# Optimization experiments

Hardware: AMD Instinct MI355X
Metric: run time of the kernel (lower is better)

## Reference

```python
import jax, jax.numpy as jnp
import numpy as np

N_HEADS = 16
HEAD_K = 128
HEAD_V = 128
SCALE_BASE = 512.0
THETA_BASE = 10000.0


def xpos_tables(seq_len, head_size):
    # Faithful to the torch xpos module with start=0, end=seq_len (no cache)
    alpha = 0.4 * head_size
    drange = np.arange(2, head_size + 2, 2, dtype=np.float32)
    theta = np.repeat((1.0 / THETA_BASE) ** (drange / head_size), 2)  # [head_size]
    zeta = np.repeat((drange / (head_size / 2) + alpha) / (1 + alpha), 2)  # [head_size]
    half = seq_len // 2
    seq = (np.arange(-half, seq_len - half, dtype=np.float32) / SCALE_BASE)[:, None, None]  # [S,1,1]
    c = np.cos(seq * theta[None, None, :])  # [S,1,head_size]
    s = np.sin(seq * theta[None, None, :])
    t = zeta[None, None, :] ** seq
    return jnp.asarray(c), jnp.asarray(s), jnp.asarray(t), jnp.asarray(1.0 / t)


def rotate_every_two(x):
    return jnp.stack((-x[..., 1::2], x[..., 0::2]), axis=-1).reshape(x.shape)


def setup_inputs() -> dict:
    key = jax.random.key(0)
    ks = jax.random.split(key, 5)
    B, S, E = 2, 2048, 2048
    return {
        "activations": jax.random.normal(ks[0], (B, S, E), dtype=jnp.float32),
        "Wq": 0.02 * jax.random.normal(ks[1], (N_HEADS * HEAD_K, E), dtype=jnp.float32),
        "Wk": 0.02 * jax.random.normal(ks[2], (N_HEADS * HEAD_K, E), dtype=jnp.float32),
        "Wv": 0.02 * jax.random.normal(ks[3], (N_HEADS * HEAD_V, E), dtype=jnp.float32),
        "Wo": 0.02 * jax.random.normal(ks[4], (E, N_HEADS * HEAD_V), dtype=jnp.float32),
    }


def reference(activations, Wq, Wk, Wv, Wo):
    B, S, E = activations.shape
    # QKV projections (torch Linear: y = x @ W.T), split heads
    q = (activations @ Wq.T).reshape(B, S, N_HEADS, HEAD_K)
    k = (activations @ Wk.T).reshape(B, S, N_HEADS, HEAD_K)
    v = (activations @ Wv.T).reshape(B, S, N_HEADS, HEAD_V)
    # xpos rotary + scale; tables have shape [S,1,head] broadcasting over heads
    c, s, t, invt = xpos_tables(S, HEAD_K)
    q = (q * c + rotate_every_two(q) * s) * t
    k = (k * c + rotate_every_two(k) * s) * invt
    # causal scaled dot-product attention
    scale = 1.0 / jnp.sqrt(jnp.float32(HEAD_K))
    scores = jnp.einsum("bqhd,bkhd->bhqk", q, k) * scale  # [B,H,S,S]
    causal = jnp.tril(jnp.ones((S, S), dtype=bool))
    scores = jnp.where(causal, scores, jnp.float32(-1e30))
    probs = jax.nn.softmax(scores, axis=-1)
    out = jnp.einsum("bhqk,bkhd->bqhd", probs, v).reshape(B, S, N_HEADS * HEAD_V)
    # down projection (dropout_rate=0 / eval mode)
    return out @ Wo.T
```

## Files before the change

### kernel.cpp

```cpp
#include <hip/hip_runtime.h>
#include <hip/hip_bf16.h>

typedef __attribute__((ext_vector_type(8))) short bf16x8;
typedef __attribute__((ext_vector_type(4))) float f32x4;
typedef __attribute__((ext_vector_type(4))) _Float16 f16x4;
typedef __attribute__((ext_vector_type(8))) _Float16 f16x8;
typedef __attribute__((ext_vector_type(4))) unsigned short u16x4;

#define B_ 2
#define S_ 2048
#define E_ 2048
#define H_ 16
#define D_ 128
#define ELEMS (B_*S_*E_)
#define WELEMS (E_*E_)

__device__ __forceinline__ unsigned short f2bf(float x) {
  unsigned int u = __float_as_uint(x);
  u += 0x7fffu + ((u >> 16) & 1u);
  return (unsigned short)(u >> 16);
}

__device__ __forceinline__ void async_load16(const void* g, void* l) {
  __builtin_amdgcn_global_load_lds(
      (const __attribute__((address_space(1))) unsigned int*)g,
      (__attribute__((address_space(3))) unsigned int*)l, 16, 0, 0);
}

__global__ __launch_bounds__(256)
void cvt_f32_bf16(const float* __restrict__ src, unsigned short* __restrict__ dst, int n4)
{
  const int i = blockIdx.x * 256 + threadIdx.x;
  if (i < n4) {
    const f32x4 v = ((const f32x4*)src)[i];
    u16x4 o;
    o.x = f2bf(v.x); o.y = f2bf(v.y); o.z = f2bf(v.z); o.w = f2bf(v.w);
    ((u16x4*)dst)[i] = o;
  }
}

__global__ __launch_bounds__(256)
void cvt4_f32_bf16(const float* __restrict__ s0, const float* __restrict__ s1,
                   const float* __restrict__ s2, const float* __restrict__ s3,
                   unsigned short* __restrict__ d0, unsigned short* __restrict__ d1,
                   unsigned short* __restrict__ d2, unsigned short* __restrict__ d3,
                   int n4)
{
  const int i = blockIdx.x * 256 + threadIdx.x;
  if (i >= n4) return;
  const float* s; unsigned short* d;
  switch (blockIdx.y) {
    case 0: s = s0; d = d0; break;
    case 1: s = s1; d = d1; break;
    case 2: s = s2; d = d2; break;
    default: s = s3; d = d3; break;
  }
  const f32x4 v = ((const f32x4*)s)[i];
  u16x4 o;
  o.x = f2bf(v.x); o.y = f2bf(v.y); o.z = f2bf(v.z); o.w = f2bf(v.w);
  ((u16x4*)d)[i] = o;
}

template<int OUTMODE>
__global__ __launch_bounds__(256)
void gemm_bt(const __hip_bfloat16* __restrict__ A,
             const __hip_bfloat16* __restrict__ Bw,
             void* __restrict__ C, int M, int N, int K)
{
  __shared__ __hip_bfloat16 As[128*32];
  __shared__ __hip_bfloat16 Bs[128*32];
  const int tid  = threadIdx.x;
  const int lane = tid & 63;
  const int w    = tid >> 6;
  const int m0 = blockIdx.y * 128;
  const int n0 = blockIdx.x * 128;
  const int wm = (w >> 1) * 64;
  const int wn = (w & 1) * 64;
  const int lrow = lane >> 2;
  const int lcol = (lane & 3) * 8;
  const int fr = lane & 15;
  const int fg = lane >> 4;

  f32x4 acc[4][4];
#pragma unroll
  for (int i = 0; i < 4; i++)
#pragma unroll
    for (int j = 0; j < 4; j++) acc[i][j] = (f32x4)0.0f;

  for (int k0 = 0; k0 < K; k0 += 32) {
    __syncthreads();
#pragma unroll
    for (int s = 0; s < 2; s++) {
      const int rbase = s*64 + w*16;
      async_load16(A  + (size_t)(m0 + rbase + lrow)*K + k0 + lcol, As + rbase*32);
      async_load16(Bw + (size_t)(n0 + rbase + lrow)*K + k0 + lcol, Bs + rbase*32);
    }
    __syncthreads();
    bf16x8 af[4], bfr[4];
#pragma unroll
    for (int i = 0; i < 4; i++) {
      af[i]  = *(const bf16x8*)(As + (wm + i*16 + fr)*32 + fg*8);
      bfr[i] = *(const bf16x8*)(Bs + (wn + i*16 + fr)*32 + fg*8);
    }
#pragma unroll
    for (int i = 0; i < 4; i++)
#pragma unroll
      for (int j = 0; j < 4; j++)
        acc[i][j] = __builtin_amdgcn_mfma_f32_16x16x32_bf16(af[i], bfr[j], acc[i][j], 0, 0, 0);
  }

#pragma unroll
  for (int i = 0; i < 4; i++) {
    const int row = m0 + wm + i*16 + fg*4;
#pragma unroll
    for (int j = 0; j < 4; j++) {
      const int col = n0 + wn + j*16 + fr;
#pragma unroll
      for (int r = 0; r < 4; r++) {
        if (OUTMODE == 1) {
          ((float*)C)[(size_t)(row + r)*N + col] = acc[i][j][r];
        } else if (OUTMODE == 0) {
          ((unsigned short*)C)[(size_t)(row + r)*N + col] = f2bf(acc[i][j][r]);
        } else if (OUTMODE == 2) {
          const int rr = row + r;
          const int b = rr >> 11, s = rr & 2047;
          const int h = col >> 7, d = col & 127;
          ((unsigned short*)C)[(((size_t)(b*H_ + h) << 11) + s)*D_ + d] = f2bf(acc[i][j][r]);
        } else {
          const int rr = row + r;
          const int b = rr >> 11, s = rr & 2047;
          const int t = col >> 11;
          const int h = (col >> 7) & 15, d = col & 127;
          ((unsigned short*)C)[(size_t)t*ELEMS +
              (((size_t)(b*H_ + h) << 11) + s)*D_ + d] = f2bf(acc[i][j][r]);
        }
      }
    }
  }
}

__global__ __launch_bounds__(256)
void xpos_rotary(__hip_bfloat16* __restrict__ Q, __hip_bfloat16* __restrict__ Kt)
{
  const int idx = blockIdx.x * 256 + threadIdx.x;
  const int j = idx & 63;
  const int s = (idx >> 6) & 2047;
  const float seq = (float)(s - 1024) * (1.0f/512.0f);
  const float dr = 2.0f + 2.0f*(float)j;
  const float theta = expf(dr * (1.0f/128.0f) * -9.210340371976184f);
  const float zeta  = (dr * (1.0f/64.0f) + 51.2f) * (1.0f/52.2f);
  const float ang = seq * theta;
  const float c  = cosf(ang);
  const float sn = sinf(ang);
  const float t  = expf(seq * logf(zeta));
  const float it = 1.0f / t;

  const size_t base = (size_t)(idx >> 6) * 128 + 2*j;
  unsigned short* Qs = (unsigned short*)Q;
  unsigned short* Ks = (unsigned short*)Kt;
  const float q0 = __bfloat162float(Q[base]),  q1 = __bfloat162float(Q[base+1]);
  Qs[base]   = f2bf((q0*c - q1*sn) * t);
  Qs[base+1] = f2bf((q1*c + q0*sn) * t);
  const float k0 = __bfloat162float(Kt[base]), k1 = __bfloat162float(Kt[base+1]);
  Ks[base]   = f2bf((k0*c - k1*sn) * it);
  Ks[base+1] = f2bf((k1*c + k0*sn) * it);
}

__global__ __launch_bounds__(256)
void transpose_v(const __hip_bfloat16* __restrict__ Vh, _Float16* __restrict__ VT3)
{
  __shared__ float tile[32][33];
  const int tx = threadIdx.x, ty = threadIdx.y;
  const int bh = blockIdx.z;
  const int s0 = blockIdx.x * 32, d0 = blockIdx.y * 32;
  const int kt = s0 >> 6, koff = s0 & 63;
#pragma unroll
  for (int r = 0; r < 4; r++) {
    const int s = s0 + ty + r*8;
    tile[ty + r*8][tx] = __bfloat162float(Vh[((size_t)bh*S_ + s)*D_ + d0 + tx]);
  }
  __syncthreads();
  const int key = koff + tx;
  const int g = (key >> 2) & 3, rr = key & 3, half = (key >> 5) & 1, s1 = (key >> 4) & 1;
  const size_t base = (size_t)bh*S_*D_ + (size_t)kt*8192 + g*16 + half*8 + s1*4 + rr;
#pragma unroll
  for (int r = 0; r < 4; r++) {
    const int d = d0 + ty + r*8;
    VT3[base + d*64] = (_Float16)tile[tx][ty + r*8];
  }
}

__global__ __launch_bounds__(256, 2)
void attn_fwd(const __hip_bfloat16* __restrict__ Qh,
              const __hip_bfloat16* __restrict__ Kh,
              const _Float16* __restrict__ VT3,
              __hip_bfloat16* __restrict__ O)
{
  __shared__ union {
    struct { unsigned short Kt[2][4096]; _Float16 Vt[2][4096]; } st;
    float ep[64*132];
  } sh;

  const int lane = threadIdx.x & 63;
  const int w    = threadIdx.x >> 6;
  const int L  = blockIdx.x;
  const int bh = (L & 7) + 8*((L >> 3) & 3);
  const int x  = 31 - (L >> 5);
  const int b = bh >> 4, h = bh & 15;
  const int q0 = x*64 + w*16;
  const int qc = lane & 15;
  const int g  = lane >> 4;
  const int qv = q0 + qc;

  const __hip_bfloat16* Kb = Kh + (size_t)bh*S_*D_;
  const _Float16* vtb = VT3 + (size_t)bh*S_*D_;

  const int kswz  = (qc & 7) << 4;
  const int vbase = qc*64 + ((g ^ ((qc >> 1) & 3)) << 4);

#define STAGE(BUF, P) do {                                                       \
    const int kb0_ = (P)*32;                                                     \
    _Pragma("unroll")                                                            \
    for (int ii = 0; ii < 2; ii++) {                                             \
      const int chunk = w*2 + ii;                                                \
      const int key   = chunk*4 + (lane >> 4);                                   \
      const int srcin = ((lane & 15)*16) ^ ((key & 7) << 4);                     \
      async_load16((const char*)Kb + (size_t)(kb0_ + key)*256 + srcin,           \
                   (char*)sh.st.Kt[BUF] + chunk*1024);                           \
    }                                                                            \
    const int kt_ = (P) >> 1, h_ = (P) & 1;                                      \
    _Pragma("unroll")                                                            \
    for (int ii = 0; ii < 2; ii++) {                                             \
      const int chunk = w*2 + ii;                                                \
      const int dd = chunk*16 + (lane >> 2);                                     \
      const int gg = (lane & 3) ^ ((lane >> 3) & 3);                             \
      async_load16((const char*)vtb + ((size_t)kt_*8192 + dd*64 + gg*16 + h_*8)*2,\
                   (char*)sh.st.Vt[BUF] + chunk*1024);                           \
    }                                                                            \
  } while (0)

#define COMPUTE(BUF, P) do {                                                     \
    const int k0_ = (P)*32;                                                      \
    const char* Kl = (const char*)sh.st.Kt[BUF];                                 \
    const char* Vl = (const char*)sh.st.Vt[BUF];                                 \
    bf16x8 ka[4], kbb[4]; f16x8 vv[8];                                           \
    _Pragma("unroll")                                                            \
    for (int c = 0; c < 4; c++) {                                                \
      const int off = (c*64 + g*16) ^ kswz;                                      \
      ka[c]  = *(const bf16x8*)(Kl + qc*256 + off);                              \
      kbb[c] = *(const bf16x8*)(Kl + (16 + qc)*256 + off);                       \
    }                                                                            \
    _Pragma("unroll")                                                            \
    for (int t = 0; t < 8; t++) vv[t] = *(const f16x8*)(Vl + t*1024 + vbase);    \
    f32x4 sA = (f32x4)0.0f, sB = (f32x4)0.0f;                                    \
    _Pragma("unroll")                                                            \
    for (int c = 0; c < 4; c++) {                                                \
      sA = __builtin_amdgcn_mfma_f32_16x16x32_bf16(ka[c],  qf[c], sA, 0, 0, 0);  \
      sB = __builtin_amdgcn_mfma_f32_16x16x32_bf16(kbb[c], qf[c], sB, 0, 0, 0);  \
    }                                                                            \
    float sv[8];                                                                 \
    _Pragma("unroll")                                                            \
    for (int r = 0; r < 4; r++) {                                                \
      sv[r]   = (k0_      + g*4 + r <= qv) ? sA[r]*scale : -1e30f;               \
      sv[4+r] = (k0_ + 16 + g*4 + r <= qv) ? sB[r]*scale : -1e30f;               \
    }                                                                            \
    float mx = sv[0];                                                            \
    _Pragma("unroll")                                                            \
    for (int j = 1; j < 8; j++) mx = fmaxf(mx, sv[j]);                           \
    mx = fmaxf(mx, __shfl_xor(mx, 16));                                          \
    mx = fmaxf(mx, __shfl_xor(mx, 32));                                          \
    const float m_new = fmaxf(m_i, mx);                                          \
    const float alpha = __expf(m_i - m_new);                                     \
    float p[8], ps = 0.0f;                                                       \
    _Pragma("unroll")                                                            \
    for (int j = 0; j < 8; j++) { p[j] = __expf(sv[j] - m_new); ps += p[j]; }    \
    ps += __shfl_xor(ps, 16);                                                    \
    ps += __shfl_xor(ps, 32);                                                    \
    l_i = l_i*alpha + ps;                                                        \
    m_i = m_new;                                                                 \
    f16x4 pA, pB;                                                                \
    _Pragma("unroll")                                                            \
    for (int r = 0; r < 4; r++) { pA[r] = (_Float16)p[r]; pB[r] = (_Float16)p[4+r]; } \
    _Pragma("unroll")                                                            \
    for (int t = 0; t < 8; t++) acc_o[t] *= alpha;                               \
    _Pragma("unroll")                                                            \
    for (int t = 0; t < 8; t++) {                                                \
      const f16x4 vA = __builtin_shufflevector(vv[t], vv[t], 0, 1, 2, 3);        \
      const f16x4 vB = __builtin_shufflevector(vv[t], vv[t], 4, 5, 6, 7);        \
      acc_o[t] = __builtin_amdgcn_mfma_f32_16x16x16f16(vA, pA, acc_o[t], 0, 0, 0); \
      acc_o[t] = __builtin_amdgcn_mfma_f32_16x16x16f16(vB, pB, acc_o[t], 0, 0, 0); \
    }                                                                            \
  } while (0)

  STAGE(0, 0);

  bf16x8 qf[4];
  {
    const __hip_bfloat16* qrow = Qh + ((size_t)bh*S_ + qv)*D_ + g*8;
#pragma unroll
    for (int c = 0; c < 4; c++) qf[c] = *(const bf16x8*)(qrow + c*32);
  }

  f32x4 acc_o[8];
#pragma unroll
  for (int t = 0; t < 8; t++) acc_o[t] = (f32x4)0.0f;
  float m_i = -1e30f, l_i = 0.0f;
  const float scale = 0.08838834764831845f;

  const int ntile = 2*x + 2;

  __syncthreads();

  for (int p = 0; p < ntile; ++p) {
    if (p + 1 < ntile) STAGE((p + 1) & 1, p + 1);
    COMPUTE(p & 1, p);
    __syncthreads();
  }

  const float inv_l = 1.0f / l_i;
#pragma unroll
  for (int t = 0; t < 8; t++)
#pragma unroll
    for (int r = 0; r < 4; r++)
      sh.ep[(w*16 + qc)*132 + t*16 + g*4 + r] = acc_o[t][r] * inv_l;
  __syncthreads();

  const int row = threadIdx.x >> 2;
  const int c0  = (threadIdx.x & 3) * 32;
  unsigned short* Os = (unsigned short*)O;
  const size_t obase = ((size_t)b*S_ + x*64 + row)*E_ + h*D_;
#pragma unroll
  for (int i = 0; i < 8; i++) {
    const f32x4 v4 = *(const f32x4*)(sh.ep + row*132 + c0 + i*4);
    u16x4 o4;
    o4.x = f2bf(v4.x); o4.y = f2bf(v4.y); o4.z = f2bf(v4.z); o4.w = f2bf(v4.w);
    *(u16x4*)(Os + obase + c0 + i*4) = o4;
  }
#undef STAGE
#undef COMPUTE
}

extern "C" void kernel_launch(void* const* d_in, const int* in_sizes, int n_in,
                              void* d_out, int out_size, void* d_ws, size_t ws_size,
                              hipStream_t stream)
{
  (void)in_sizes; (void)n_in; (void)out_size; (void)ws_size;
  const float* act = (const float*)d_in[0];
  const float* Wq  = (const float*)d_in[1];
  const float* Wk  = (const float*)d_in[2];
  const float* Wv  = (const float*)d_in[3];
  const float* Wo  = (const float*)d_in[4];

  __hip_bfloat16* actb = (__hip_bfloat16*)d_ws;
  __hip_bfloat16* Wqb  = actb + ELEMS;
  __hip_bfloat16* Wkb  = Wqb + WELEMS;
  __hip_bfloat16* Wvb  = Wkb + WELEMS;
  __hip_bfloat16* Wob  = Wvb + WELEMS;
  __hip_bfloat16* Q    = Wob + WELEMS;
  __hip_bfloat16* Kp   = Q + ELEMS;
  __hip_bfloat16* V    = Kp + ELEMS;
  _Float16*       VT   = (_Float16*)(V + ELEMS);
  __hip_bfloat16* AO   = V;

  cvt_f32_bf16<<<ELEMS/4/256, 256, 0, stream>>>(act, (unsigned short*)actb, ELEMS/4);
  cvt4_f32_bf16<<<dim3(WELEMS/4/256, 4), 256, 0, stream>>>(
      Wq, Wk, Wv, Wo,
      (unsigned short*)Wqb, (unsigned short*)Wkb,
      (unsigned short*)Wvb, (unsigned short*)Wob, WELEMS/4);

  const dim3 gq(3*E_/128, (B_*S_)/128);
  gemm_bt<3><<<gq, 256, 0, stream>>>(actb, Wqb, Q, B_*S_, 3*E_, E_);

  xpos_rotary<<<(B_*S_*H_*64)/256, 256, 0, stream>>>(Q, Kp);
  transpose_v<<<dim3(S_/32, D_/32, B_*H_), dim3(32, 8), 0, stream>>>(V, VT);
  attn_fwd<<<1024, 256, 0, stream>>>(Q, Kp, VT, AO);

  const dim3 gg(E_/128, (B_*S_)/128);
  gemm_bt<1><<<gg, 256, 0, stream>>>(AO, Wob, d_out, B_*S_, E_, E_);
}
```

Before: 437.5 us.

## Add 256x256 eight-wave pipelined GEMM for the fused QKV projection

Adds a new bf16 GEMM kernel with 256x256 output tiles, 512 threads, double-buffered 128KB LDS filled by async global-to-LDS loads, XOR-swizzled LDS layout, an XCD-aware block swizzle, and interleaved barrier/priority scheduling of MFMA against the next tile's loads. The QKV projection now uses it instead of the 128x128 kernel. The goal is more data reuse per tile and better overlap of memory traffic with matrix-core work. The cost is high register and LDS pressure, and the large dynamic LDS request may limit occupancy or fail to launch if the attribute is not set.

```diff
diff --git a/kernel.cpp b/kernel.cpp
--- a/kernel.cpp
+++ b/kernel.cpp
@@ -139,6 +139,175 @@
   }
 }
 
+template<int OUTMODE>
+__global__ __launch_bounds__(512, 2)
+void gemm_bt8(const __hip_bfloat16* __restrict__ A,
+              const __hip_bfloat16* __restrict__ Bw,
+              void* __restrict__ C, int M, int N, int K)
+{
+  extern __shared__ char lds[];
+  const int tid  = threadIdx.x;
+  const int lane = tid & 63;
+  const int w    = tid >> 6;
+  const int fr   = lane & 15;
+  const int fg   = lane >> 4;
+
+  const int nblk = N >> 8;
+  const int cpx  = gridDim.x >> 3;
+  const int lin  = blockIdx.x;
+  const int swz  = (lin & 7) * cpx + (lin >> 3);
+  const int m0 = (swz / nblk) << 8;
+  const int n0 = (swz % nblk) << 8;
+
+  const int Ssw = (fg ^ (fr & 3)) << 4;
+  const int pA  = ((w >> 2) * 128 + fr) * 64 + Ssw;
+  const int pB  = 32768 + ((w & 3) * 64 + fr) * 64 + Ssw;
+
+  const int r0 = w * 32 + (lane >> 2);
+  const int ks = ((lane & 3) ^ ((lane >> 2) & 3)) * 8;
+  const __hip_bfloat16* Asrc = A  + (size_t)(m0 + r0) * K + ks;
+  const __hip_bfloat16* Bsrc = Bw + (size_t)(n0 + r0) * K + ks;
+  const int dgrp = w * 2048;
+
+#define STG(NB, OPB, KH, KT) do {                                              \
+    const size_t ko_ = (size_t)(KT)*64 + (KH)*32;                              \
+    const __hip_bfloat16* sp_ = (OPB) ? Bsrc : Asrc;                           \
+    char* dp_ = lds + (NB)*65536 + (OPB)*32768 + (KH)*16384 + dgrp;            \
+    async_load16(sp_ + ko_, dp_);                                              \
+    async_load16(sp_ + (size_t)16*K + ko_, dp_ + 1024);                        \
+  } while (0)
+
+#define RDA(DST, KK, BB, MI0) do {                                             \
+    const char* p_ = lds + (BB)*65536 + (KK)*16384 + pA + (MI0)*1024;          \
+    DST[0] = *(const bf16x8*)(p_);                                             \
+    DST[1] = *(const bf16x8*)(p_ + 1024);                                      \
+    DST[2] = *(const bf16x8*)(p_ + 2048);                                      \
+    DST[3] = *(const bf16x8*)(p_ + 3072);                                      \
+  } while (0)
+
+#define RDB(DST, KK, BB) do {                                                  \
+    const char* p_ = lds + (BB)*65536 + (KK)*16384 + pB;                       \
+    DST[0] = *(const bf16x8*)(p_);                                             \
+    DST[1] = *(const bf16x8*)(p_ + 1024);                                      \
+    DST[2] = *(const bf16x8*)(p_ + 2048);                                      \
+    DST[3] = *(const bf16x8*)(p_ + 3072);                                      \
+  } while (0)
+
+#define MFMA16(MI0, AR, BR)                                                    \
+    _Pragma("unroll")                                                          \
+    for (int i_ = 0; i_ < 4; i_++)                                             \
+    _Pragma("unroll")                                                          \
+    for (int j_ = 0; j_ < 4; j_++)                                             \
+      acc[(MI0)+i_][j_] = __builtin_amdgcn_mfma_f32_16x16x32_bf16(             \
+          AR[i_], BR[j_], acc[(MI0)+i_][j_], 0, 0, 0)
+
+#define BARX() __builtin_amdgcn_s_barrier()
+#define LGKM0() do { asm volatile("s_waitcnt lgkmcnt(0)" ::: "memory");        \
+                     __builtin_amdgcn_sched_barrier(0); } while (0)
+#define VMW(NN) asm volatile("s_waitcnt vmcnt(" #NN ")" ::: "memory")
+#define PRIO(P) __builtin_amdgcn_s_setprio(P)
+
+  f32x4 acc[8][4];
+#pragma unroll
+  for (int i = 0; i < 8; i++)
+#pragma unroll
+    for (int j = 0; j < 4; j++) acc[i][j] = (f32x4)0.0f;
+
+  STG(0, 0, 0, 0);
+  STG(0, 1, 0, 0);
+  STG(0, 0, 1, 0);
+  STG(0, 1, 1, 0);
+  VMW(4);
+  BARX();
+
+  const int nk = K >> 6;
+  bf16x8 aR[4], bR[4];
+
+  for (int t = 0; t < nk - 1; ++t) {
+    const int bb = t & 1, nb = bb ^ 1;
+    RDA(aR, 0, bb, 0); RDB(bR, 0, bb);
+    STG(nb, 0, 0, t + 1);
+    BARX(); LGKM0();
+    PRIO(1); MFMA16(0, aR, bR); PRIO(0);
+    BARX();
+    RDA(aR, 0, bb, 4);
+    STG(nb, 1, 0, t + 1);
+    BARX(); LGKM0();
+    PRIO(1); MFMA16(4, aR, bR); PRIO(0);
+    VMW(4);
+    BARX();
+    RDA(aR, 1, bb, 0); RDB(bR, 1, bb);
+    STG(nb, 0, 1, t + 1);
+    BARX(); LGKM0();
+    PRIO(1); MFMA16(0, aR, bR); PRIO(0);
+    BARX();
+    RDA(aR, 1, bb, 4);
+    STG(nb, 1, 1, t + 1);
+    BARX(); LGKM0();
+    PRIO(1); MFMA16(4, aR, bR); PRIO(0);
+    VMW(4);
+    BARX();
+  }
+  {
+    const int bb = (nk - 1) & 1;
+    RDA(aR, 0, bb, 0); RDB(bR, 0, bb);
+    BARX(); LGKM0();
+    PRIO(1); MFMA16(0, aR, bR); PRIO(0);
+    BARX();
+    RDA(aR, 0, bb, 4);
+    BARX(); LGKM0();
+    PRIO(1); MFMA16(4, aR, bR); PRIO(0);
+    VMW(0);
+    BARX();
+    RDA(aR, 1, bb, 0); RDB(bR, 1, bb);
+    BARX(); LGKM0();
+    PRIO(1); MFMA16(0, aR, bR); PRIO(0);
+    BARX();
+    RDA(aR, 1, bb, 4);
+    BARX(); LGKM0();
+    PRIO(1); MFMA16(4, aR, bR); PRIO(0);
+    BARX();
+  }
+
+  const int wr = (w >> 2) * 128, wc = (w & 3) * 64;
+#pragma unroll
+  for (int mi = 0; mi < 8; mi++) {
+    const int row = m0 + wr + mi*16 + fg*4;
+#pragma unroll
+    for (int nj = 0; nj < 4; nj++) {
+      const int col = n0 + wc + nj*16 + fr;
+#pragma unroll
+      for (int r = 0; r < 4; r++) {
+        if (OUTMODE == 1) {
+          ((float*)C)[(size_t)(row + r)*N + col] = acc[mi][nj][r];
+        } else if (OUTMODE == 0) {
+          ((unsigned short*)C)[(size_t)(row + r)*N + col] = f2bf(acc[mi][nj][r]);
+        } else if (OUTMODE == 2) {
+          const int rr = row + r;
+          const int b = rr >> 11, s = rr & 2047;
+          const int h = col >> 7, d = col & 127;
+          ((unsigned short*)C)[(((size_t)(b*H_ + h) << 11) + s)*D_ + d] = f2bf(acc[mi][nj][r]);
+        } else {
+          const int rr = row + r;
+          const int b = rr >> 11, s = rr & 2047;
+          const int t = col >> 11;
+          const int h = (col >> 7) & 15, d = col & 127;
+          ((unsigned short*)C)[(size_t)t*ELEMS +
+              (((size_t)(b*H_ + h) << 11) + s)*D_ + d] = f2bf(acc[mi][nj][r]);
+        }
+      }
+    }
+  }
+#undef STG
+#undef RDA
+#undef RDB
+#undef MFMA16
+#undef BARX
+#undef LGKM0
+#undef VMW
+#undef PRIO
+}
+
 __global__ __launch_bounds__(256)
 void xpos_rotary(__hip_bfloat16* __restrict__ Q, __hip_bfloat16* __restrict__ Kt)
 {
@@ -368,8 +537,8 @@
       (unsigned short*)Wqb, (unsigned short*)Wkb,
       (unsigned short*)Wvb, (unsigned short*)Wob, WELEMS/4);
 
-  const dim3 gq(3*E_/128, (B_*S_)/128);
-  gemm_bt<3><<<gq, 256, 0, stream>>>(actb, Wqb, Q, B_*S_, 3*E_, E_);
+  gemm_bt8<3><<<(B_*S_/256)*(3*E_/256), 512, 131072, stream>>>(
+      actb, Wqb, Q, B_*S_, 3*E_, E_);
 
   xpos_rotary<<<(B_*S_*H_*64)/256, 256, 0, stream>>>(Q, Kp);
   transpose_v<<<dim3(S_/32, D_/32, B_*H_), dim3(32, 8), 0, stream>>>(V, VT);
```

New measurement: 411.4 us. -6.0%, faster.

## Replace GEMM with double-buffered 256x128 tile kernel using swizzled LDS

Applied to the files above, without the earlier changes.

Replaces the simple 128x128, single-buffer bf16 GEMM with a 512-thread kernel that computes a 256x128 tile and uses a K-step of 64. Global-to-LDS async loads go into a double buffer so the next tile loads while the current one is multiplied. It also adds an XOR-swizzled LDS layout against bank conflicts, a grouped block-index swizzle for L2 reuse, and s_setprio around the MFMA bursts. The cost is 96KB of dynamic LDS per block and fragile hand-placed waitcnt and barrier ordering.

```diff
diff --git a/kernel.cpp b/kernel.cpp
--- a/kernel.cpp
+++ b/kernel.cpp
@@ -62,24 +62,66 @@
 }
 
 template<int OUTMODE>
-__global__ __launch_bounds__(256)
-void gemm_bt(const __hip_bfloat16* __restrict__ A,
-             const __hip_bfloat16* __restrict__ Bw,
-             void* __restrict__ C, int M, int N, int K)
-{
-  __shared__ __hip_bfloat16 As[128*32];
-  __shared__ __hip_bfloat16 Bs[128*32];
-  const int tid  = threadIdx.x;
-  const int lane = tid & 63;
-  const int w    = tid >> 6;
-  const int m0 = blockIdx.y * 128;
-  const int n0 = blockIdx.x * 128;
-  const int wm = (w >> 1) * 64;
-  const int wn = (w & 1) * 64;
-  const int lrow = lane >> 2;
-  const int lcol = (lane & 3) * 8;
-  const int fr = lane & 15;
-  const int fg = lane >> 4;
+__global__ __launch_bounds__(512, 2)
+void gemm_bt9(const __hip_bfloat16* __restrict__ A,
+              const __hip_bfloat16* __restrict__ Bw,
+              void* __restrict__ C, int M, int N, int K)
+{
+  extern __shared__ char lds[];
+  const int lane = threadIdx.x & 63;
+  const int w    = threadIdx.x >> 6;
+  const int fr   = lane & 15;
+  const int fg   = lane >> 4;
+
+  const int nblk = N >> 7;
+  const int cpx  = gridDim.x >> 3;
+  const int lin  = blockIdx.x;
+  const int swz  = (lin & 7) * cpx + (lin >> 3);
+  const int m0 = (swz / nblk) << 8;
+  const int n0 = (swz % nblk) << 7;
+
+  const int Ssw = (fg ^ ((fr >> 1) & 3)) << 4;
+  const int pA  = ((w >> 1) * 64 + fr) * 64 + Ssw;
+  const int pB  = 32768 + ((w & 1) * 64 + fr) * 64 + Ssw;
+
+  const int srow = w * 16 + (lane >> 2);
+  const int ks   = ((lane & 3) ^ ((lane >> 3) & 3)) * 8;
+  const __hip_bfloat16* Asrc = A  + (size_t)(m0 + srow) * K + ks;
+  const __hip_bfloat16* Bsrc = Bw + (size_t)(n0 + srow) * K + ks;
+  const int dstA = srow * 64 + (lane & 3) * 16;
+
+#define STG(NB, KH, KT) do {                                                   \
+    const size_t ko_ = (size_t)(KT)*64 + (KH)*32;                              \
+    async_load16(Asrc + ko_,                                                   \
+                 lds + (NB)*49152 + (KH)*16384 + dstA);                        \
+    async_load16(Asrc + (size_t)128*K + ko_,                                   \
+                 lds + (NB)*49152 + (KH)*16384 + 8192 + dstA);                 \
+    async_load16(Bsrc + ko_,                                                   \
+                 lds + (NB)*49152 + 32768 + (KH)*8192 + dstA);                 \
+  } while (0)
+
+#define RD(KK, BB) do {                                                        \
+    const char* pa_ = lds + (BB)*49152 + (KK)*16384 + pA;                      \
+    aR[0] = *(const bf16x8*)(pa_);        aR[1] = *(const bf16x8*)(pa_ + 1024);\
+    aR[2] = *(const bf16x8*)(pa_ + 2048); aR[3] = *(const bf16x8*)(pa_ + 3072);\
+    const char* pb_ = lds + (BB)*49152 + (KK)*8192 + pB;                       \
+    bR[0] = *(const bf16x8*)(pb_);        bR[1] = *(const bf16x8*)(pb_ + 1024);\
+    bR[2] = *(const bf16x8*)(pb_ + 2048); bR[3] = *(const bf16x8*)(pb_ + 3072);\
+  } while (0)
+
+#define MFMA16()                                                               \
+    _Pragma("unroll")                                                          \
+    for (int i_ = 0; i_ < 4; i_++)                                             \
+    _Pragma("unroll")                                                          \
+    for (int j_ = 0; j_ < 4; j_++)                                             \
+      acc[i_][j_] = __builtin_amdgcn_mfma_f32_16x16x32_bf16(                   \
+          aR[i_], bR[j_], acc[i_][j_], 0, 0, 0)
+
+#define BARX() __builtin_amdgcn_s_barrier()
+#define LGKM0() do { asm volatile("s_waitcnt lgkmcnt(0)" ::: "memory");        \
+                     __builtin_amdgcn_sched_barrier(0); } while (0)
+#define VMW(NN) asm volatile("s_waitcnt vmcnt(" #NN ")" ::: "memory")
+#define PRIO(P) __builtin_amdgcn_s_setprio(P)
 
   f32x4 acc[4][4];
 #pragma unroll
@@ -87,56 +129,78 @@
 #pragma unroll
     for (int j = 0; j < 4; j++) acc[i][j] = (f32x4)0.0f;
 
-  for (int k0 = 0; k0 < K; k0 += 32) {
-    __syncthreads();
-#pragma unroll
-    for (int s = 0; s < 2; s++) {
-      const int rbase = s*64 + w*16;
-      async_load16(A  + (size_t)(m0 + rbase + lrow)*K + k0 + lcol, As + rbase*32);
-      async_load16(Bw + (size_t)(n0 + rbase + lrow)*K + k0 + lcol, Bs + rbase*32);
-    }
-    __syncthreads();
-    bf16x8 af[4], bfr[4];
-#pragma unroll
-    for (int i = 0; i < 4; i++) {
-      af[i]  = *(const bf16x8*)(As + (wm + i*16 + fr)*32 + fg*8);
-      bfr[i] = *(const bf16x8*)(Bs + (wn + i*16 + fr)*32 + fg*8);
-    }
-#pragma unroll
-    for (int i = 0; i < 4; i++)
-#pragma unroll
-      for (int j = 0; j < 4; j++)
-        acc[i][j] = __builtin_amdgcn_mfma_f32_16x16x32_bf16(af[i], bfr[j], acc[i][j], 0, 0, 0);
-  }
-
-#pragma unroll
-  for (int i = 0; i < 4; i++) {
-    const int row = m0 + wm + i*16 + fg*4;
-#pragma unroll
-    for (int j = 0; j < 4; j++) {
-      const int col = n0 + wn + j*16 + fr;
+  bf16x8 aR[4], bR[4];
+
+  STG(0, 0, 0);
+  STG(0, 1, 0);
+  VMW(3);
+  BARX();
+
+  const int nk = K >> 6;
+
+  for (int t = 0; t < nk - 1; ++t) {
+    const int bb = t & 1, nb = bb ^ 1;
+    RD(0, bb);
+    STG(nb, 0, t + 1);
+    BARX(); LGKM0();
+    PRIO(1); MFMA16(); PRIO(0);
+    VMW(3);
+    BARX();
+    RD(1, bb);
+    STG(nb, 1, t + 1);
+    BARX(); LGKM0();
+    PRIO(1); MFMA16(); PRIO(0);
+    VMW(3);
+    BARX();
+  }
+  {
+    const int bb = (nk - 1) & 1;
+    RD(0, bb);
+    BARX(); LGKM0();
+    PRIO(1); MFMA16(); PRIO(0);
+    VMW(0);
+    BARX();
+    RD(1, bb);
+    BARX(); LGKM0();
+    PRIO(1); MFMA16(); PRIO(0);
+  }
+
+  const int wr = (w >> 1) * 64, wc = (w & 1) * 64;
+#pragma unroll
+  for (int mi = 0; mi < 4; mi++) {
+    const int row = m0 + wr + mi*16 + fg*4;
+#pragma unroll
+    for (int nj = 0; nj < 4; nj++) {
+      const int col = n0 + wc + nj*16 + fr;
 #pragma unroll
       for (int r = 0; r < 4; r++) {
         if (OUTMODE == 1) {
-          ((float*)C)[(size_t)(row + r)*N + col] = acc[i][j][r];
+          ((float*)C)[(size_t)(row + r)*N + col] = acc[mi][nj][r];
         } else if (OUTMODE == 0) {
-          ((unsigned short*)C)[(size_t)(row + r)*N + col] = f2bf(acc[i][j][r]);
+          ((unsigned short*)C)[(size_t)(row + r)*N + col] = f2bf(acc[mi][nj][r]);
         } else if (OUTMODE == 2) {
           const int rr = row + r;
           const int b = rr >> 11, s = rr & 2047;
           const int h = col >> 7, d = col & 127;
-          ((unsigned short*)C)[(((size_t)(b*H_ + h) << 11) + s)*D_ + d] = f2bf(acc[i][j][r]);
+          ((unsigned short*)C)[(((size_t)(b*H_ + h) << 11) + s)*D_ + d] = f2bf(acc[mi][nj][r]);
         } else {
           const int rr = row + r;
           const int b = rr >> 11, s = rr & 2047;
-          const int t = col >> 11;
+          const int t2 = col >> 11;
           const int h = (col >> 7) & 15, d = col & 127;
-          ((unsigned short*)C)[(size_t)t*ELEMS +
-              (((size_t)(b*H_ + h) << 11) + s)*D_ + d] = f2bf(acc[i][j][r]);
+          ((unsigned short*)C)[(size_t)t2*ELEMS +
+              (((size_t)(b*H_ + h) << 11) + s)*D_ + d] = f2bf(acc[mi][nj][r]);
         }
       }
     }
   }
+#undef STG
+#undef RD
+#undef MFMA16
+#undef BARX
+#undef LGKM0
+#undef VMW
+#undef PRIO
 }
 
 __global__ __launch_bounds__(256)
@@ -368,13 +432,13 @@
       (unsigned short*)Wqb, (unsigned short*)Wkb,
       (unsigned short*)Wvb, (unsigned short*)Wob, WELEMS/4);
 
-  const dim3 gq(3*E_/128, (B_*S_)/128);
-  gemm_bt<3><<<gq, 256, 0, stream>>>(actb, Wqb, Q, B_*S_, 3*E_, E_);
+  gemm_bt9<3><<<(B_*S_/256)*(3*E_/128), 512, 98304, stream>>>(
+      actb, Wqb, Q, B_*S_, 3*E_, E_);
 
   xpos_rotary<<<(B_*S_*H_*64)/256, 256, 0, stream>>>(Q, Kp);
   transpose_v<<<dim3(S_/32, D_/32, B_*H_), dim3(32, 8), 0, stream>>>(V, VT);
   attn_fwd<<<1024, 256, 0, stream>>>(Q, Kp, VT, AO);
 
-  const dim3 gg(E_/128, (B_*S_)/128);
-  gemm_bt<1><<<gg, 256, 0, stream>>>(AO, Wob, d_out, B_*S_, E_, E_);
-}
+  gemm_bt9<1><<<(B_*S_/256)*(E_/128), 512, 98304, stream>>>(
+      AO, Wob, d_out, B_*S_, E_, E_);
+}
```

Result: faster. 400.1 us (-8.6%).
